# Kernel optimization log

Hardware: AMD Instinct MI355X
Metric: run time of the kernel (lower is better)

The kernel has to match this reference:

```python
import jax, jax.numpy as jnp
import numpy as np

C = 1.0          # curvature
ALPHA = 0.2      # LeakyReLU negative slope
MIN_NORM = 1e-15
MASK_VAL = -9e15

def artanh(x):
    x = jnp.clip(x, -1 + 1e-7, 1 - 1e-7)
    return 0.5 * (jnp.log1p(x) - jnp.log1p(-x))

def logmap0(x, c):
    sqrt_c = jnp.sqrt(c)
    norm = jnp.maximum(jnp.linalg.norm(x, axis=-1, keepdims=True), MIN_NORM)
    return x / (sqrt_c * norm) * artanh(sqrt_c * norm)

def expmap0(u, c):
    sqrt_c = jnp.sqrt(c)
    norm = jnp.maximum(jnp.linalg.norm(u, axis=-1, keepdims=True), MIN_NORM)
    return jnp.tanh(sqrt_c * norm) * u / (sqrt_c * norm)

def proj(x, c):
    norm = jnp.maximum(jnp.linalg.norm(x, axis=-1, keepdims=True), MIN_NORM)
    maxnorm = (1.0 - 1e-5) / jnp.sqrt(c)
    return jnp.where(norm > maxnorm, x / norm * maxnorm, x)

def setup_inputs() -> dict:
    key = jax.random.key(0)
    k1, k2, k3, k4, k5 = jax.random.split(key, 5)
    N, D, CLS = 8192, 128, 16
    # points on the Poincare ball (small norm, then projected)
    x = proj(jax.random.normal(k1, (N, D), jnp.float32) * 0.01, C)
    # sparse-ish adjacency, avg degree ~32, with self loops
    adj = jax.random.uniform(k2, (N, N)) < (32.0 / N)
    adj = adj | jnp.eye(N, dtype=bool)
    W = jax.random.normal(k3, (D, CLS), jnp.float32) * (1.0 / np.sqrt(D))
    b = jnp.zeros((CLS,), jnp.float32)
    a_src = jax.random.normal(k4, (CLS,), jnp.float32) * 0.1
    a_dst = jax.random.normal(k5, (CLS,), jnp.float32) * 0.1
    return {"x": x, "adj": adj, "W": W, "b": b, "a_src": a_src, "a_dst": a_dst}

def reference(x, adj, W, b, a_src, a_dst):
    # hyperbolic -> tangent space at origin, then linear map to n_classes
    h = logmap0(x, C) @ W + b                              # [N, CLS]
    # GAT scores: e_ij = LeakyReLU(a_src.h_i + a_dst.h_j)
    e = jax.nn.leaky_relu((h @ a_src)[:, None] + (h @ a_dst)[None, :], ALPHA)  # [N, N]
    e = jnp.where(adj, e, MASK_VAL)
    att = jax.nn.softmax(e, axis=-1)                       # row softmax over neighbors
    out = jax.nn.elu(att @ h)                              # aggregate + activation
    # back onto the manifold
    return proj(expmap0(out, C), C)
```

## Files before the change

### kernel.cpp

```cpp
#include <hip/hip_runtime.h>
#include <math.h>

#define NN  8192
#define DD  128
#define CLS 16
#define ALPHA 0.2f

__global__ void adj_probe(const unsigned char* __restrict__ adj, int* flag)
{
    const int lane = threadIdx.x & 63;
    const int i = lane + 1;
    const int ok = ((i & 3) != 0) && (adj[(size_t)i * (NN + 1)] != 0);
    unsigned long long b = __ballot(ok);
    if (threadIdx.x == 0) *flag = (__popcll(b) > 24) ? 1 : 0;
}

__global__ __launch_bounds__(256) void hat_feat(
    const float* __restrict__ x, const float* __restrict__ W,
    const float* __restrict__ b, const float* __restrict__ a_src,
    const float* __restrict__ a_dst,
    float* __restrict__ h, float* __restrict__ s, float* __restrict__ dv)
{
    const int lane = threadIdx.x & 63;
    const int row  = (blockIdx.x << 2) + (threadIdx.x >> 6);

    const float* xr = x + (size_t)row * DD;
    float x0 = xr[lane];
    float x1 = xr[lane + 64];

    float nsq = x0 * x0 + x1 * x1;
    #pragma unroll
    for (int o = 32; o > 0; o >>= 1) nsq += __shfl_xor(nsq, o);

    float norm = fmaxf(sqrtf(nsq), 1e-15f);
    float t    = fminf(norm, 1.0f - 1e-7f);
    float art  = 0.5f * (log1pf(t) - log1pf(-t));
    float scl  = art / norm;
    x0 *= scl;
    x1 *= scl;

    float hc[CLS];
    #pragma unroll
    for (int c = 0; c < CLS; ++c)
        hc[c] = x0 * W[lane * CLS + c] + x1 * W[(lane + 64) * CLS + c];

    #pragma unroll
    for (int o = 32; o > 0; o >>= 1) {
        #pragma unroll
        for (int c = 0; c < CLS; ++c) hc[c] += __shfl_xor(hc[c], o);
    }

    float sv = 0.0f, dvv = 0.0f;
    #pragma unroll
    for (int c = 0; c < CLS; ++c) {
        hc[c] += b[c];
        sv  += hc[c] * a_src[c];
        dvv += hc[c] * a_dst[c];
    }

    if (lane == 0) {
        float* hr = h + (size_t)row * CLS;
        #pragma unroll
        for (int c = 0; c < CLS; ++c) hr[c] = hc[c];
        s[row]  = sv;
        dv[row] = dvv;
    }
}

__global__ __launch_bounds__(256) void hat_attn(
    const float* __restrict__ h, const float* __restrict__ s,
    const float* __restrict__ dv, const unsigned char* __restrict__ adj,
    const int* __restrict__ flag, float* __restrict__ out)
{
    const int lane = threadIdx.x & 63;
    const int row  = (blockIdx.x << 2) + (threadIdx.x >> 6);
    const int cc   = lane & 15;

    const float si = s[row];
    float m = -3.0e38f, l = 0.0f, acc = 0.0f;

    auto hit = [&](int j) {
        float e = si + dv[j];
        e = (e > 0.0f) ? e : ALPHA * e;
        float hv = h[(size_t)j * CLS + cc];
        if (e <= m) {
            float w = __expf(e - m);
            l += w;
            acc = fmaf(w, hv, acc);
        } else {
            float sc = __expf(m - e);
            l   = fmaf(l, sc, 1.0f);
            acc = fmaf(acc, sc, hv);
            m = e;
        }
    };

    if (*flag) {
        const uint4* arow = reinterpret_cast<const uint4*>(adj + (size_t)row * NN);
        #pragma unroll
        for (int it = 0; it < 8; ++it) {
            const uint4 a = arow[(it << 6) | lane];
            const int S = it << 10;
            unsigned n0 = ((a.x & 0x01010101u) * 0x01020408u) >> 24;
            unsigned n1 = ((a.y & 0x01010101u) * 0x01020408u) >> 24;
            unsigned n2 = ((a.z & 0x01010101u) * 0x01020408u) >> 24;
            unsigned n3 = ((a.w & 0x01010101u) * 0x01020408u) >> 24;
            unsigned pm = (n0 & 0xF) | ((n1 & 0xF) << 4)
                        | ((n2 & 0xF) << 8) | ((n3 & 0xF) << 12);
            #pragma unroll
            for (int k = 0; k < 16; ++k) {
                unsigned long long bmask = __ballot((pm >> k) & 1u);
                while (bmask) {
                    const int t = __builtin_ctzll(bmask);
                    bmask &= bmask - 1;
                    hit(S + (t << 4) + k);
                }
            }
        }
    } else {
        const uint4* arow = reinterpret_cast<const uint4*>(
            reinterpret_cast<const unsigned int*>(adj) + (size_t)row * NN);
        for (int it = 0; it < 32; ++it) {
            const uint4 a = arow[(it << 6) | lane];
            const int S = it << 8;
            #pragma unroll
            for (int k = 0; k < 4; ++k) {
                const unsigned v = (&a.x)[k];
                unsigned long long bmask = __ballot(v != 0u);
                while (bmask) {
                    const int t = __builtin_ctzll(bmask);
                    bmask &= bmask - 1;
                    hit(S + (t << 2) + k);
                }
            }
        }
    }

    float* orow = out + (size_t)row * CLS;
    if (l > 0.0f) {
        float u = acc / l;
        u = (u > 0.0f) ? u : expm1f(u);
        float nsq = u * u;
        #pragma unroll
        for (int o = 8; o > 0; o >>= 1) nsq += __shfl_xor(nsq, o);
        float norm = fmaxf(sqrtf(nsq), 1e-15f);
        float th   = tanhf(norm);
        float sc2  = th / norm;
        const float maxnorm = 1.0f - 1e-5f;
        float sc3  = (th > maxnorm) ? (maxnorm / th) : 1.0f;
        if (lane < CLS) orow[lane] = u * sc2 * sc3;
    } else {
        if (lane < CLS) orow[lane] = 0.0f;
    }
}

extern "C" void kernel_launch(void* const* d_in, const int* in_sizes, int n_in,
                              void* d_out, int out_size, void* d_ws, size_t ws_size,
                              hipStream_t stream) {
    const float*         x     = (const float*)d_in[0];
    const unsigned char* adj   = (const unsigned char*)d_in[1];
    const float*         W     = (const float*)d_in[2];
    const float*         b     = (const float*)d_in[3];
    const float*         a_src = (const float*)d_in[4];
    const float*         a_dst = (const float*)d_in[5];
    float*               out   = (float*)d_out;

    float* h    = (float*)d_ws;
    float* s    = h + (size_t)NN * CLS;
    float* dv   = s + NN;
    int*   flag = (int*)(dv + NN);

    adj_probe<<<1, 64, 0, stream>>>(adj, flag);
    hat_feat<<<NN / 4, 256, 0, stream>>>(x, W, b, a_src, a_dst, h, s, dv);
    hat_attn<<<NN / 4, 256, 0, stream>>>(h, s, dv, adj, flag, out);
}
```

Before: 67.25 us.

## Build per-lane neighbor bitmasks and inline adjacency format probe into attention kernel

Removes the separate adj_probe launch; each wave now runs the format probe inline. The attention kernel first loads the whole adjacency row and packs each lane's neighbor bits into two 64-bit masks. It then walks only lanes with set bits, broadcasting their masks with shuffles, instead of issuing 16 or 4 ballots per load iteration. The intent is fewer ballot and loop-control steps, one fewer kernel launch, and all row loads issued up front. The cost is a redundant probe per wave and extra shuffles per active lane.

New measurement: 81.31 us. 20.9% more time.

```diff
diff --git a/kernel.cpp b/kernel.cpp
--- a/kernel.cpp
+++ b/kernel.cpp
@@ -5,15 +5,6 @@
 #define DD  128
 #define CLS 16
 #define ALPHA 0.2f
-
-__global__ void adj_probe(const unsigned char* __restrict__ adj, int* flag)
-{
-    const int lane = threadIdx.x & 63;
-    const int i = lane + 1;
-    const int ok = ((i & 3) != 0) && (adj[(size_t)i * (NN + 1)] != 0);
-    unsigned long long b = __ballot(ok);
-    if (threadIdx.x == 0) *flag = (__popcll(b) > 24) ? 1 : 0;
-}
 
 __global__ __launch_bounds__(256) void hat_feat(
     const float* __restrict__ x, const float* __restrict__ W,
@@ -70,11 +61,46 @@
 __global__ __launch_bounds__(256) void hat_attn(
     const float* __restrict__ h, const float* __restrict__ s,
     const float* __restrict__ dv, const unsigned char* __restrict__ adj,
-    const int* __restrict__ flag, float* __restrict__ out)
+    float* __restrict__ out)
 {
     const int lane = threadIdx.x & 63;
     const int row  = (blockIdx.x << 2) + (threadIdx.x >> 6);
     const int cc   = lane & 15;
+
+    {
+    }
+    const int pi = lane + 1;
+    const int pok = ((pi & 3) != 0) && (adj[(size_t)pi * (NN + 1)] != 0);
+    const bool bytemode = __popcll(__ballot(pok)) > 24;
+
+    unsigned long long m0 = 0ull, m1 = 0ull;
+    if (bytemode) {
+        const uint4* arow = reinterpret_cast<const uint4*>(adj + (size_t)row * NN);
+        #pragma unroll
+        for (int it = 0; it < 8; ++it) {
+            const uint4 a = arow[(it << 6) | lane];
+            unsigned n0 = ((a.x & 0x01010101u) * 0x01020408u) >> 24;
+            unsigned n1 = ((a.y & 0x01010101u) * 0x01020408u) >> 24;
+            unsigned n2 = ((a.z & 0x01010101u) * 0x01020408u) >> 24;
+            unsigned n3 = ((a.w & 0x01010101u) * 0x01020408u) >> 24;
+            unsigned long long bits = (unsigned long long)(
+                (n0 & 0xF) | ((n1 & 0xF) << 4) | ((n2 & 0xF) << 8) | ((n3 & 0xF) << 12));
+            if (it < 4) m0 |= bits << (it << 4);
+            else        m1 |= bits << ((it - 4) << 4);
+        }
+    } else {
+        const uint4* arow = reinterpret_cast<const uint4*>(
+            reinterpret_cast<const unsigned int*>(adj) + (size_t)row * NN);
+        #pragma unroll
+        for (int it = 0; it < 32; ++it) {
+            const uint4 a = arow[(it << 6) | lane];
+            unsigned long long bits =
+                (unsigned long long)((a.x != 0u) | ((a.y != 0u) << 1) |
+                                     ((a.z != 0u) << 2) | ((a.w != 0u) << 3));
+            if (it < 16) m0 |= bits << (it << 2);
+            else         m1 |= bits << ((it - 16) << 2);
+        }
+    }
 
     const float si = s[row];
     float m = -3.0e38f, l = 0.0f, acc = 0.0f;
@@ -95,44 +121,26 @@
         }
     };
 
-    if (*flag) {
-        const uint4* arow = reinterpret_cast<const uint4*>(adj + (size_t)row * NN);
-        #pragma unroll
-        for (int it = 0; it < 8; ++it) {
-            const uint4 a = arow[(it << 6) | lane];
-            const int S = it << 10;
-            unsigned n0 = ((a.x & 0x01010101u) * 0x01020408u) >> 24;
-            unsigned n1 = ((a.y & 0x01010101u) * 0x01020408u) >> 24;
-            unsigned n2 = ((a.z & 0x01010101u) * 0x01020408u) >> 24;
-            unsigned n3 = ((a.w & 0x01010101u) * 0x01020408u) >> 24;
-            unsigned pm = (n0 & 0xF) | ((n1 & 0xF) << 4)
-                        | ((n2 & 0xF) << 8) | ((n3 & 0xF) << 12);
-            #pragma unroll
-            for (int k = 0; k < 16; ++k) {
-                unsigned long long bmask = __ballot((pm >> k) & 1u);
-                while (bmask) {
-                    const int t = __builtin_ctzll(bmask);
-                    bmask &= bmask - 1;
-                    hit(S + (t << 4) + k);
-                }
-            }
+    auto decode = [&](int t, int b) -> int {
+        return bytemode ? (((b >> 4) << 10) | (t << 4) | (b & 15))
+                        : (((b >> 2) << 8)  | (t << 2) | (b & 3));
+    };
+
+    unsigned long long act = __ballot((m0 | m1) != 0ull);
+    while (act) {
+        const int t = __builtin_ctzll(act);
+        act &= act - 1;
+        unsigned long long mm0 = __shfl(m0, t);
+        unsigned long long mm1 = __shfl(m1, t);
+        while (mm0) {
+            const int b = __builtin_ctzll(mm0);
+            mm0 &= mm0 - 1;
+            hit(decode(t, b));
         }
-    } else {
-        const uint4* arow = reinterpret_cast<const uint4*>(
-            reinterpret_cast<const unsigned int*>(adj) + (size_t)row * NN);
-        for (int it = 0; it < 32; ++it) {
-            const uint4 a = arow[(it << 6) | lane];
-            const int S = it << 8;
-            #pragma unroll
-            for (int k = 0; k < 4; ++k) {
-                const unsigned v = (&a.x)[k];
-                unsigned long long bmask = __ballot(v != 0u);
-                while (bmask) {
-                    const int t = __builtin_ctzll(bmask);
-                    bmask &= bmask - 1;
-                    hit(S + (t << 2) + k);
-                }
-            }
+        while (mm1) {
+            const int b = __builtin_ctzll(mm1);
+            mm1 &= mm1 - 1;
+            hit(decode(t, b + 64));
         }
     }
 
@@ -165,12 +173,10 @@
     const float*         a_dst = (const float*)d_in[5];
     float*               out   = (float*)d_out;
 
-    float* h    = (float*)d_ws;
-    float* s    = h + (size_t)NN * CLS;
-    float* dv   = s + NN;
-    int*   flag = (int*)(dv + NN);
+    float* h  = (float*)d_ws;
+    float* s  = h + (size_t)NN * CLS;
+    float* dv = s + NN;
 
-    adj_probe<<<1, 64, 0, stream>>>(adj, flag);
     hat_feat<<<NN / 4, 256, 0, stream>>>(x, W, b, a_src, a_dst, h, s, dv);
-    hat_attn<<<NN / 4, 256, 0, stream>>>(h, s, dv, adj, flag, out);
+    hat_attn<<<NN / 4, 256, 0, stream>>>(h, s, dv, adj, out);
 }
```

## Split attention into adjacency compaction pass and parallel aggregation pass

Applied to the files above, without the earlier changes.

Replaces the single attention kernel, which walked neighbors one at a time with a ballot-driven online softmax, with two kernels. The first scans each adjacency row into a bitmask, prefix-sums the per-lane counts and writes a compacted neighbor index list (capped at MAXD). The second does a two-pass softmax: a parallel max over neighbors, then four neighbor groups per wave accumulating weights across the class lanes, followed by a shuffle reduction. This removes the serial per-hit dependency and branchy online rescaling. The cost is an extra launch, writing and re-reading the index list, and silently truncating any row with more than 1024 neighbors.

After: 72.20 us. 7.4% more time.

```diff
diff --git a/kernel.cpp b/kernel.cpp
--- a/kernel.cpp
+++ b/kernel.cpp
@@ -1,10 +1,11 @@
 #include <hip/hip_runtime.h>
 #include <math.h>
 
-#define NN  8192
-#define DD  128
-#define CLS 16
+#define NN   8192
+#define DD   128
+#define CLS  16
 #define ALPHA 0.2f
+#define MAXD 1024
 
 __global__ void adj_probe(const unsigned char* __restrict__ adj, int* flag)
 {
@@ -67,74 +68,112 @@
     }
 }
 
-__global__ __launch_bounds__(256) void hat_attn(
-    const float* __restrict__ h, const float* __restrict__ s,
-    const float* __restrict__ dv, const unsigned char* __restrict__ adj,
-    const int* __restrict__ flag, float* __restrict__ out)
+__global__ __launch_bounds__(256) void hat_scan(
+    const unsigned char* __restrict__ adj, const int* __restrict__ flag,
+    int* __restrict__ nbr, int* __restrict__ cnt)
 {
     const int lane = threadIdx.x & 63;
     const int row  = (blockIdx.x << 2) + (threadIdx.x >> 6);
-    const int cc   = lane & 15;
-
-    const float si = s[row];
-    float m = -3.0e38f, l = 0.0f, acc = 0.0f;
-
-    auto hit = [&](int j) {
-        float e = si + dv[j];
-        e = (e > 0.0f) ? e : ALPHA * e;
-        float hv = h[(size_t)j * CLS + cc];
-        if (e <= m) {
-            float w = __expf(e - m);
-            l += w;
-            acc = fmaf(w, hv, acc);
-        } else {
-            float sc = __expf(m - e);
-            l   = fmaf(l, sc, 1.0f);
-            acc = fmaf(acc, sc, hv);
-            m = e;
-        }
-    };
-
-    if (*flag) {
+    const bool bytemode = (*flag != 0);
+
+    unsigned long long m0 = 0ull, m1 = 0ull;
+    if (bytemode) {
         const uint4* arow = reinterpret_cast<const uint4*>(adj + (size_t)row * NN);
         #pragma unroll
         for (int it = 0; it < 8; ++it) {
             const uint4 a = arow[(it << 6) | lane];
-            const int S = it << 10;
             unsigned n0 = ((a.x & 0x01010101u) * 0x01020408u) >> 24;
             unsigned n1 = ((a.y & 0x01010101u) * 0x01020408u) >> 24;
             unsigned n2 = ((a.z & 0x01010101u) * 0x01020408u) >> 24;
             unsigned n3 = ((a.w & 0x01010101u) * 0x01020408u) >> 24;
-            unsigned pm = (n0 & 0xF) | ((n1 & 0xF) << 4)
-                        | ((n2 & 0xF) << 8) | ((n3 & 0xF) << 12);
-            #pragma unroll
-            for (int k = 0; k < 16; ++k) {
-                unsigned long long bmask = __ballot((pm >> k) & 1u);
-                while (bmask) {
-                    const int t = __builtin_ctzll(bmask);
-                    bmask &= bmask - 1;
-                    hit(S + (t << 4) + k);
-                }
-            }
+            unsigned long long bits = (unsigned long long)(
+                (n0 & 0xF) | ((n1 & 0xF) << 4) | ((n2 & 0xF) << 8) | ((n3 & 0xF) << 12));
+            if (it < 4) m0 |= bits << (it << 4);
+            else        m1 |= bits << ((it - 4) << 4);
         }
     } else {
         const uint4* arow = reinterpret_cast<const uint4*>(
             reinterpret_cast<const unsigned int*>(adj) + (size_t)row * NN);
+        #pragma unroll
         for (int it = 0; it < 32; ++it) {
             const uint4 a = arow[(it << 6) | lane];
-            const int S = it << 8;
-            #pragma unroll
-            for (int k = 0; k < 4; ++k) {
-                const unsigned v = (&a.x)[k];
-                unsigned long long bmask = __ballot(v != 0u);
-                while (bmask) {
-                    const int t = __builtin_ctzll(bmask);
-                    bmask &= bmask - 1;
-                    hit(S + (t << 2) + k);
-                }
-            }
+            unsigned long long bits =
+                (unsigned long long)((a.x != 0u) | ((a.y != 0u) << 1) |
+                                     ((a.z != 0u) << 2) | ((a.w != 0u) << 3));
+            if (it < 16) m0 |= bits << (it << 2);
+            else         m1 |= bits << ((it - 16) << 2);
         }
     }
+
+    const int c = __popcll(m0) + __popcll(m1);
+    int off = c;
+    #pragma unroll
+    for (int o = 1; o < 64; o <<= 1) {
+        int v = __shfl_up(off, o);
+        if (lane >= o) off += v;
+    }
+    const int total = __shfl(off, 63);
+    off -= c;
+
+    int* rbase = nbr + (size_t)row * MAXD;
+    while (m0) {
+        const int b = __builtin_ctzll(m0);
+        m0 &= m0 - 1;
+        const int j = bytemode ? (((b >> 4) << 10) | (lane << 4) | (b & 15))
+                               : (((b >> 2) << 8)  | (lane << 2) | (b & 3));
+        if (off < MAXD) rbase[off] = j;
+        ++off;
+    }
+    while (m1) {
+        const int b0 = __builtin_ctzll(m1);
+        m1 &= m1 - 1;
+        const int b = b0 + 64;
+        const int j = bytemode ? (((b >> 4) << 10) | (lane << 4) | (b & 15))
+                               : (((b >> 2) << 8)  | (lane << 2) | (b & 3));
+        if (off < MAXD) rbase[off] = j;
+        ++off;
+    }
+    if (lane == 0) cnt[row] = (total < MAXD) ? total : MAXD;
+}
+
+__global__ __launch_bounds__(256) void hat_agg(
+    const float* __restrict__ h, const float* __restrict__ s,
+    const float* __restrict__ dv, const int* __restrict__ nbr,
+    const int* __restrict__ cnt, float* __restrict__ out)
+{
+    const int lane = threadIdx.x & 63;
+    const int row  = (blockIdx.x << 2) + (threadIdx.x >> 6);
+    const int cc   = lane & 15;
+    const int g    = lane >> 4;
+
+    const int n = cnt[row];
+    const int* rbase = nbr + (size_t)row * MAXD;
+    const float si = s[row];
+
+    float mx = -3.0e38f;
+    for (int i = lane; i < n; i += 64) {
+        float e = si + dv[rbase[i]];
+        e = (e > 0.0f) ? e : ALPHA * e;
+        mx = fmaxf(mx, e);
+    }
+    #pragma unroll
+    for (int o = 32; o > 0; o >>= 1) mx = fmaxf(mx, __shfl_xor(mx, o));
+
+    float l = 0.0f, acc = 0.0f;
+    #pragma unroll 2
+    for (int base = 0; base < n; base += 4) {
+        const int idx = base + g;
+        if (idx < n) {
+            const int j = rbase[idx];
+            float e = si + dv[j];
+            e = (e > 0.0f) ? e : ALPHA * e;
+            const float w = __expf(e - mx);
+            l += w;
+            acc = fmaf(w, h[(size_t)j * CLS + cc], acc);
+        }
+    }
+    l   += __shfl_xor(l, 16);   l   += __shfl_xor(l, 32);
+    acc += __shfl_xor(acc, 16); acc += __shfl_xor(acc, 32);
 
     float* orow = out + (size_t)row * CLS;
     if (l > 0.0f) {
@@ -169,8 +208,11 @@
     float* s    = h + (size_t)NN * CLS;
     float* dv   = s + NN;
     int*   flag = (int*)(dv + NN);
+    int*   cnt  = flag + 1;
+    int*   nbr  = cnt + NN;
 
     adj_probe<<<1, 64, 0, stream>>>(adj, flag);
     hat_feat<<<NN / 4, 256, 0, stream>>>(x, W, b, a_src, a_dst, h, s, dv);
-    hat_attn<<<NN / 4, 256, 0, stream>>>(h, s, dv, adj, flag, out);
-}
+    hat_scan<<<NN / 4, 256, 0, stream>>>(adj, flag, nbr, cnt);
+    hat_agg <<<NN / 4, 256, 0, stream>>>(h, s, dv, nbr, cnt, out);
+}
```
